# Kernel tuning notes

Hardware: AMD Instinct MI355X
Metric: run time of the kernel (lower is better)

## Reference

```python
import jax, jax.numpy as jnp
import numpy as np

N = 50000       # nodes
E = 800000      # edges (avg degree 16)
F_IN = 128      # num_node_features
H = 128         # hidden_dim
C = 16          # num_classes
G = 512         # graphs in batch


def setup_inputs() -> dict:
    key = jax.random.key(0)
    ks = jax.random.split(key, 12)
    x = jax.random.normal(ks[0], (N, F_IN), dtype=jnp.float32)
    edge_index = jax.random.randint(ks[1], (2, E), 0, N, dtype=jnp.int32)
    batch = jnp.sort(jax.random.randint(ks[2], (N,), 0, G, dtype=jnp.int32))
    def lin(k, fan_in, shape):
        bound = 1.0 / np.sqrt(fan_in)
        return jax.random.uniform(k, shape, jnp.float32, -bound, bound)
    # SAGEConv1: lin_l (aggr, with bias), lin_r (root, no bias)
    w1l = lin(ks[3], F_IN, (F_IN, H)); b1 = lin(ks[4], F_IN, (H,))
    w1r = lin(ks[5], F_IN, (F_IN, H))
    # SAGEConv2
    w2l = lin(ks[6], H, (H, H)); b2 = lin(ks[7], H, (H,))
    w2r = lin(ks[8], H, (H, H))
    # final fc
    wf = lin(ks[9], H, (H, C)); bf = lin(ks[10], H, (C,))
    return {"x": x, "edge_index": edge_index, "batch": batch,
            "w1l": w1l, "b1": b1, "w1r": w1r,
            "w2l": w2l, "b2": b2, "w2r": w2r,
            "wf": wf, "bf": bf}


def _sage_conv(x, src, dst, wl, bl, wr):
    # mean-aggregate source-node features at destination nodes
    msg_sum = jax.ops.segment_sum(x[src], dst, num_segments=N)      # [N, d]
    cnt = jax.ops.segment_sum(jnp.ones((src.shape[0], 1), x.dtype), dst,
                              num_segments=N)                        # [N, 1]
    aggr = msg_sum / jnp.maximum(cnt, 1.0)
    return aggr @ wl + bl + x @ wr


def reference(x, edge_index, batch, w1l, b1, w1r, w2l, b2, w2r, wf, bf):
    src, dst = edge_index[0], edge_index[1]
    h = jax.nn.relu(_sage_conv(x, src, dst, w1l, b1, w1r))
    # dropout(p=0.5) is identity at inference
    h = jax.nn.relu(_sage_conv(h, src, dst, w2l, b2, w2r))
    # global_mean_pool over graph ids
    gsum = jax.ops.segment_sum(h, batch, num_segments=G)             # [G, H]
    gcnt = jax.ops.segment_sum(jnp.ones((N, 1), h.dtype), batch,
                               num_segments=G)                        # [G, 1]
    g = gsum / jnp.maximum(gcnt, 1.0)
    logits = g @ wf + bf
    return jax.nn.log_softmax(logits, axis=1)
```

## Files before the change

kernel.cpp:

```cpp
#include <hip/hip_runtime.h>
#include <hip/hip_bf16.h>
#include <math.h>


#define FDIM 128

typedef __attribute__((ext_vector_type(8))) short bf16x8;
typedef __attribute__((ext_vector_type(4))) float f32x4;

__device__ inline unsigned short f2bf(float f) {
    union { float f; unsigned u; } v; v.f = f;
    unsigned r = v.u + 0x7fff + ((v.u >> 16) & 1);
    return (unsigned short)(r >> 16);
}
__device__ inline float bf2f(unsigned short b) {
    union { unsigned u; float f; } v; v.u = ((unsigned)b) << 16;
    return v.f;
}

__device__ inline void acc8(float* a, uint4 w) {
    union { unsigned u; float f; } t;
    t.u = w.x << 16;          a[0] += t.f;
    t.u = w.x & 0xffff0000u;  a[1] += t.f;
    t.u = w.y << 16;          a[2] += t.f;
    t.u = w.y & 0xffff0000u;  a[3] += t.f;
    t.u = w.z << 16;          a[4] += t.f;
    t.u = w.z & 0xffff0000u;  a[5] += t.f;
    t.u = w.w << 16;          a[6] += t.f;
    t.u = w.w & 0xffff0000u;  a[7] += t.f;
}
__device__ inline void acc8m(float* a, uint4 w, float m) {
    union { unsigned u; float f; } t;
    t.u = w.x << 16;          a[0] = fmaf(m, t.f, a[0]);
    t.u = w.x & 0xffff0000u;  a[1] = fmaf(m, t.f, a[1]);
    t.u = w.y << 16;          a[2] = fmaf(m, t.f, a[2]);
    t.u = w.y & 0xffff0000u;  a[3] = fmaf(m, t.f, a[3]);
    t.u = w.z << 16;          a[4] = fmaf(m, t.f, a[4]);
    t.u = w.z & 0xffff0000u;  a[5] = fmaf(m, t.f, a[5]);
    t.u = w.w << 16;          a[6] = fmaf(m, t.f, a[6]);
    t.u = w.w & 0xffff0000u;  a[7] = fmaf(m, t.f, a[7]);
}

__global__ __launch_bounds__(256) void prep_k(
        const int* __restrict__ dst, int* __restrict__ deg, int* __restrict__ rank, int nE,
        const float* __restrict__ x, unsigned short* __restrict__ xb, int n4,
        const float* __restrict__ w1l, const float* __restrict__ w1r,
        unsigned short* __restrict__ wp1,
        const float* __restrict__ w2l, const float* __restrict__ w2r,
        unsigned short* __restrict__ wp2,
        int nbE, int nbC) {
    int bid = blockIdx.x, tid = threadIdx.x;
    if (bid < nbE) {
        int e = bid * 256 + tid;
        if (e < nE) rank[e] = atomicAdd(&deg[dst[e]], 1);
    } else if (bid < nbE + nbC) {
        int i = (bid - nbE) * 256 + tid;
        if (i < n4) {
            float4 v = ((const float4*)x)[i];
            ushort4 o;
            o.x = f2bf(v.x); o.y = f2bf(v.y); o.z = f2bf(v.z); o.w = f2bf(v.w);
            ((ushort4*)xb)[i] = o;
        }
    } else {
        int pb = bid - nbE - nbC;
        const float* wl = (pb < 16) ? w1l : w2l;
        const float* wr = (pb < 16) ? w1r : w2r;
        unsigned short* wp = (pb < 16) ? wp1 : wp2;
        int t = (pb & 15) * 256 + tid;
        int lane = t & 63, s = (t >> 6) & 7, nt = t >> 9;
        int kbase = s * 32 + ((lane >> 4) * 8);
        int c = nt * 16 + (lane & 15);
        unsigned short tmp[8];
        #pragma unroll
        for (int j = 0; j < 8; ++j) {
            int k = kbase + j;
            float w = (k < 128) ? wl[k * 128 + c] : wr[(k - 128) * 128 + c];
            tmp[j] = f2bf(w);
        }
        ushort4 lo, hi;
        lo.x = tmp[0]; lo.y = tmp[1]; lo.z = tmp[2]; lo.w = tmp[3];
        hi.x = tmp[4]; hi.y = tmp[5]; hi.z = tmp[6]; hi.w = tmp[7];
        ((ushort4*)wp)[t * 2 + 0] = lo;
        ((ushort4*)wp)[t * 2 + 1] = hi;
    }
}

__global__ __launch_bounds__(256) void scan1_k(const int* __restrict__ deg,
                                               int* __restrict__ rowstart,
                                               int* __restrict__ bsum, int n) {
    __shared__ int s[256];
    int tid = threadIdx.x;
    int i = blockIdx.x * 256 + tid;
    int v = (i < n) ? deg[i] : 0;
    s[tid] = v;
    __syncthreads();
    for (int off = 1; off < 256; off <<= 1) {
        int t = (tid >= off) ? s[tid - off] : 0;
        __syncthreads();
        s[tid] += t;
        __syncthreads();
    }
    if (i < n) rowstart[i] = s[tid] - v;
    if (tid == 255) bsum[blockIdx.x] = s[255];
}

__global__ __launch_bounds__(256) void scan2_k(int* __restrict__ bsum, int nb) {
    __shared__ int s[256];
    int tid = threadIdx.x;
    int v = (tid < nb) ? bsum[tid] : 0;
    s[tid] = v;
    __syncthreads();
    for (int off = 1; off < 256; off <<= 1) {
        int t = (tid >= off) ? s[tid - off] : 0;
        __syncthreads();
        s[tid] += t;
        __syncthreads();
    }
    if (tid < nb) bsum[tid] = s[tid] - v;
}

__global__ void addoff_k(int* __restrict__ rowstart, const int* __restrict__ bsum, int n) {
    int i = blockIdx.x * blockDim.x + threadIdx.x;
    if (i < n) rowstart[i] += bsum[blockIdx.x];
}

__global__ __launch_bounds__(256) void fill_swz_k(
        const int* __restrict__ src, const int* __restrict__ dst,
        const int* __restrict__ rowstart, const int* __restrict__ rank,
        int* __restrict__ csr, int nE, int rngSize) {
    int cls = blockIdx.x & 7;
    int lo = cls * rngSize, hi = lo + rngSize;
    int nb = gridDim.x >> 3;
    int bi = blockIdx.x >> 3;
    for (int e = bi * 256 + threadIdx.x; e < nE; e += nb * 256) {
        int d = dst[e];
        if (d >= lo && d < hi)
            csr[rowstart[d] + rank[e]] = src[e];
    }
}

__global__ __launch_bounds__(256) void gather_v4_k(
        const uint4* __restrict__ feat,
        const int* __restrict__ csr, const int* __restrict__ rowstart,
        const int* __restrict__ deg, uint4* __restrict__ outr, int n) {
    int node = blockIdx.x * 4 + (threadIdx.x >> 6);
    if (node >= n) return;
    int lane = threadIdx.x & 63;
    int es = lane >> 4;
    int cs = lane & 15;
    int s0 = rowstart[node], dc = deg[node];

    float acc[8] = {0.f, 0.f, 0.f, 0.f, 0.f, 0.f, 0.f, 0.f};
    int base = 0;
    int i0 = 0, i1 = 0, i2 = 0, i3 = 0;
    if (base + 16 <= dc) {
        i0 = csr[s0 + es];
        i1 = csr[s0 + 4 + es];
        i2 = csr[s0 + 8 + es];
        i3 = csr[s0 + 12 + es];
    }
    while (base + 16 <= dc) {
        uint4 w0 = feat[(size_t)i0 * 16 + cs];
        uint4 w1 = feat[(size_t)i1 * 16 + cs];
        uint4 w2 = feat[(size_t)i2 * 16 + cs];
        uint4 w3 = feat[(size_t)i3 * 16 + cs];
        base += 16;
        if (base + 16 <= dc) {
            i0 = csr[s0 + base + es];
            i1 = csr[s0 + base + 4 + es];
            i2 = csr[s0 + base + 8 + es];
            i3 = csr[s0 + base + 12 + es];
        }
        acc8(acc, w0);
        acc8(acc, w1);
        acc8(acc, w2);
        acc8(acc, w3);
    }
    if (base < dc) {
        int c = dc - 1;
        int e0 = base + es, e1 = base + 4 + es, e2 = base + 8 + es, e3 = base + 12 + es;
        int t0 = csr[s0 + min(e0, c)];
        int t1 = csr[s0 + min(e1, c)];
        int t2 = csr[s0 + min(e2, c)];
        int t3 = csr[s0 + min(e3, c)];
        uint4 w0 = feat[(size_t)t0 * 16 + cs];
        uint4 w1 = feat[(size_t)t1 * 16 + cs];
        uint4 w2 = feat[(size_t)t2 * 16 + cs];
        uint4 w3 = feat[(size_t)t3 * 16 + cs];
        acc8m(acc, w0, (e0 < dc) ? 1.0f : 0.0f);
        acc8m(acc, w1, (e1 < dc) ? 1.0f : 0.0f);
        acc8m(acc, w2, (e2 < dc) ? 1.0f : 0.0f);
        acc8m(acc, w3, (e3 < dc) ? 1.0f : 0.0f);
    }

    #pragma unroll
    for (int k = 0; k < 8; ++k) {
        acc[k] += __shfl_xor(acc[k], 16, 64);
        acc[k] += __shfl_xor(acc[k], 32, 64);
    }

    if (es == 0) {
        float inv = (dc > 0) ? 1.0f / (float)dc : 0.0f;
        uint4 o;
        o.x = ((unsigned)f2bf(acc[1] * inv) << 16) | (unsigned)f2bf(acc[0] * inv);
        o.y = ((unsigned)f2bf(acc[3] * inv) << 16) | (unsigned)f2bf(acc[2] * inv);
        o.z = ((unsigned)f2bf(acc[5] * inv) << 16) | (unsigned)f2bf(acc[4] * inv);
        o.w = ((unsigned)f2bf(acc[7] * inv) << 16) | (unsigned)f2bf(acc[6] * inv);
        outr[(size_t)node * 16 + cs] = o;
    }
}

__global__ __launch_bounds__(256) void gemm_mfma_k(
        const unsigned short* __restrict__ A,
        const unsigned short* __restrict__ R,
        const unsigned short* __restrict__ wp,
        const float* __restrict__ bias,
        unsigned short* __restrict__ outp,
        int n) {
    int tid = threadIdx.x;
    int wave = tid >> 6, lane = tid & 63;
    int rowTile = blockIdx.x * 64 + wave * 16;
    int lrow = lane & 15, lk = lane >> 4;

    int arow = rowTile + lrow;
    if (arow >= n) arow = n - 1;

    bf16x8 a[8];
    const unsigned short* abase = A + (size_t)arow * FDIM + lk * 8;
    const unsigned short* rbase = R + (size_t)arow * FDIM + lk * 8;
    #pragma unroll
    for (int s = 0; s < 4; ++s) a[s] = *(const bf16x8*)(abase + s * 32);
    #pragma unroll
    for (int s = 0; s < 4; ++s) a[4 + s] = *(const bf16x8*)(rbase + s * 32);

    const bf16x8* bp = (const bf16x8*)wp;
    int ocol = lane & 15;
    int orow0 = rowTile + (lane >> 4) * 4;

    #pragma unroll
    for (int nt = 0; nt < 8; ++nt) {
        float bv = bias[nt * 16 + ocol];
        f32x4 acc = {bv, bv, bv, bv};
        #pragma unroll
        for (int s = 0; s < 8; ++s) {
            bf16x8 b = bp[(nt * 8 + s) * 64 + lane];
            acc = __builtin_amdgcn_mfma_f32_16x16x32_bf16(a[s], b, acc, 0, 0, 0);
        }
        #pragma unroll
        for (int r = 0; r < 4; ++r) {
            int orow = orow0 + r;
            if (orow < n) {
                float v = fmaxf(acc[r], 0.0f);
                outp[(size_t)orow * FDIM + nt * 16 + ocol] = f2bf(v);
            }
        }
    }
}

__global__ __launch_bounds__(256) void pool_seg_k(
        const unsigned short* __restrict__ h,
        const int* __restrict__ batch,
        float* __restrict__ gsum, int* __restrict__ gcnt, int nN) {
    __shared__ int bw[64];
    __shared__ float red[8][32][4];
    int base = blockIdx.x * 64;
    if (base >= nN) return;
    int tid = threadIdx.x;
    int rg = tid >> 5, cs = tid & 31;
    int cnt = min(64, nN - base);
    if (tid < 64) bw[tid] = batch[min(base + tid, nN - 1)];
    __syncthreads();
    int g0 = bw[0], g1 = bw[cnt - 1];

    for (int g = g0; g <= g1; ++g) {
        int s = 0;
        while (s < cnt && bw[s] < g) ++s;
        int e = s;
        while (e < cnt && bw[e] == g) ++e;

        float a0 = 0.f, a1 = 0.f, a2 = 0.f, a3 = 0.f;
        for (int i = s + rg; i < e; i += 8) {
            uint2 v = ((const uint2*)(h + (size_t)(base + i) * FDIM))[cs];
            a0 += bf2f((unsigned short)(v.x & 0xffff));
            a1 += bf2f((unsigned short)(v.x >> 16));
            a2 += bf2f((unsigned short)(v.y & 0xffff));
            a3 += bf2f((unsigned short)(v.y >> 16));
        }
        red[rg][cs][0] = a0; red[rg][cs][1] = a1;
        red[rg][cs][2] = a2; red[rg][cs][3] = a3;
        __syncthreads();
        if (rg == 0 && e > s) {
            #pragma unroll
            for (int r = 1; r < 8; ++r) {
                a0 += red[r][cs][0]; a1 += red[r][cs][1];
                a2 += red[r][cs][2]; a3 += red[r][cs][3];
            }
            float* go = gsum + (size_t)g * FDIM + cs * 4;
            atomicAdd(go + 0, a0);
            atomicAdd(go + 1, a1);
            atomicAdd(go + 2, a2);
            atomicAdd(go + 3, a3);
            if (cs == 0) atomicAdd(&gcnt[g], e - s);
        }
        __syncthreads();
    }
}

__global__ __launch_bounds__(128) void head_k(const float* __restrict__ gsum,
                                              const int* __restrict__ gcnt,
                                              const float* __restrict__ wf,
                                              const float* __restrict__ bf,
                                              float* __restrict__ out, int nG) {
    int g = blockIdx.x;
    if (g >= nG) return;
    __shared__ float row[FDIM];
    int tid = threadIdx.x;
    float inv = 1.0f / fmaxf((float)gcnt[g], 1.0f);
    row[tid] = gsum[(size_t)g * FDIM + tid] * inv;
    __syncthreads();

    float logit = -1e30f;
    if (tid < 16) {
        logit = bf[tid];
        for (int k = 0; k < FDIM; ++k) logit += row[k] * wf[k * 16 + tid];
    }
    float m = logit;
    for (int off = 8; off >= 1; off >>= 1) m = fmaxf(m, __shfl_xor(m, off, 64));
    float ev = (tid < 16) ? expf(logit - m) : 0.0f;
    float sum = ev;
    for (int off = 8; off >= 1; off >>= 1) sum += __shfl_xor(sum, off, 64);
    if (tid < 16) out[(size_t)g * 16 + tid] = logit - m - logf(sum);
}

extern "C" void kernel_launch(void* const* d_in, const int* in_sizes, int n_in,
                              void* d_out, int out_size, void* d_ws, size_t ws_size,
                              hipStream_t stream) {
    const float* x    = (const float*)d_in[0];
    const int*   ei   = (const int*)d_in[1];
    const int*   batch= (const int*)d_in[2];
    const float* w1l  = (const float*)d_in[3];
    const float* b1   = (const float*)d_in[4];
    const float* w1r  = (const float*)d_in[5];
    const float* w2l  = (const float*)d_in[6];
    const float* b2   = (const float*)d_in[7];
    const float* w2r  = (const float*)d_in[8];
    const float* wf   = (const float*)d_in[9];
    const float* bf   = (const float*)d_in[10];
    float* out = (float*)d_out;

    const int N = in_sizes[0] / FDIM;
    const int E = in_sizes[1] / 2;
    const int G = out_size / 16;
    const int* src = ei;
    const int* dst = ei + E;
    const int NB = (N + 255) / 256;

    char* ws = (char*)d_ws;
    size_t off = 0;
    auto alloc = [&](size_t bytes) { void* p = ws + off; off = (off + bytes + 255) & ~(size_t)255; return p; };
    unsigned short* xb   = (unsigned short*)alloc((size_t)N * FDIM * 2);
    unsigned short* aggr = (unsigned short*)alloc((size_t)N * FDIM * 2);
    unsigned short* h1   = (unsigned short*)alloc((size_t)N * FDIM * 2);
    unsigned short* wp1  = (unsigned short*)alloc(8 * 8 * 64 * 8 * 2);
    unsigned short* wp2  = (unsigned short*)alloc(8 * 8 * 64 * 8 * 2);
    int* deg      = (int*)alloc((size_t)N * sizeof(int));
    int* rowstart = (int*)alloc((size_t)N * sizeof(int));
    int* bsum     = (int*)alloc(256 * sizeof(int));
    int* csr      = (int*)alloc((size_t)E * sizeof(int));
    int* rank     = (int*)alloc((size_t)E * sizeof(int));
    float* gsum   = (float*)alloc((size_t)G * FDIM * sizeof(float));
    int*   gcnt   = (int*)alloc((size_t)G * sizeof(int));
    unsigned short* h2 = xb;

    hipMemsetAsync(deg, 0, (size_t)N * sizeof(int), stream);
    hipMemsetAsync(gsum, 0, (size_t)G * FDIM * sizeof(float), stream);
    hipMemsetAsync(gcnt, 0, (size_t)G * sizeof(int), stream);

    const int nbE = (E + 255) / 256;
    const int nbC = (N * FDIM / 4 + 255) / 256;
    prep_k<<<nbE + nbC + 32, 256, 0, stream>>>(dst, deg, rank, E,
                                               x, xb, N * FDIM / 4,
                                               w1l, w1r, wp1, w2l, w2r, wp2,
                                               nbE, nbC);

    scan1_k<<<NB, 256, 0, stream>>>(deg, rowstart, bsum, N);
    scan2_k<<<1, 256, 0, stream>>>(bsum, NB);
    addoff_k<<<NB, 256, 0, stream>>>(rowstart, bsum, N);
    {
        int rngSize = (N + 7) / 8;
        fill_swz_k<<<2048, 256, 0, stream>>>(src, dst, rowstart, rank, csr, E, rngSize);
    }

    gather_v4_k<<<(N + 3) / 4, 256, 0, stream>>>((const uint4*)xb, csr, rowstart, deg,
                                                 (uint4*)aggr, N);
    gemm_mfma_k<<<(N + 63) / 64, 256, 0, stream>>>(aggr, xb, wp1, b1, h1, N);

    gather_v4_k<<<(N + 3) / 4, 256, 0, stream>>>((const uint4*)h1, csr, rowstart, deg,
                                                 (uint4*)aggr, N);
    gemm_mfma_k<<<(N + 63) / 64, 256, 0, stream>>>(aggr, h1, wp2, b2, h2, N);

    pool_seg_k<<<(N + 63) / 64, 256, 0, stream>>>(h2, batch, gsum, gcnt, N);
    head_k<<<G, 128, 0, stream>>>(gsum, gcnt, wf, bf, out, G);
}
```

Before: 177.1 us.

## Build CSR with per-node atomic cursors instead of stored edge ranks

Removes the per-edge rank array: degree counting moves into a separate swizzled kernel where each block handles one destination range, and the CSR fill claims slots with atomicAdd on a per-node cursor initialised from rowstart. This drops the rank write and read and should keep atomics local to one XCD range. In exchange the degree count no longer overlaps with the x conversion in one launch, adds a kernel launch, and makes neighbour order within a row nondeterministic, so float summation order can vary between runs.

```diff
diff --git a/kernel.cpp b/kernel.cpp
--- a/kernel.cpp
+++ b/kernel.cpp
@@ -42,19 +42,15 @@
 }
 
 __global__ __launch_bounds__(256) void prep_k(
-        const int* __restrict__ dst, int* __restrict__ deg, int* __restrict__ rank, int nE,
         const float* __restrict__ x, unsigned short* __restrict__ xb, int n4,
         const float* __restrict__ w1l, const float* __restrict__ w1r,
         unsigned short* __restrict__ wp1,
         const float* __restrict__ w2l, const float* __restrict__ w2r,
         unsigned short* __restrict__ wp2,
-        int nbE, int nbC) {
+        int nbC) {
     int bid = blockIdx.x, tid = threadIdx.x;
-    if (bid < nbE) {
-        int e = bid * 256 + tid;
-        if (e < nE) rank[e] = atomicAdd(&deg[dst[e]], 1);
-    } else if (bid < nbE + nbC) {
-        int i = (bid - nbE) * 256 + tid;
+    if (bid < nbC) {
+        int i = bid * 256 + tid;
         if (i < n4) {
             float4 v = ((const float4*)x)[i];
             ushort4 o;
@@ -62,7 +58,7 @@
             ((ushort4*)xb)[i] = o;
         }
     } else {
-        int pb = bid - nbE - nbC;
+        int pb = bid - nbC;
         const float* wl = (pb < 16) ? w1l : w2l;
         const float* wr = (pb < 16) ? w1r : w2r;
         unsigned short* wp = (pb < 16) ? wp1 : wp2;
@@ -85,6 +81,18 @@
     }
 }
 
+__global__ __launch_bounds__(256) void deg_swz_k(
+        const int* __restrict__ dst, int* __restrict__ deg, int nE, int rngSize) {
+    int cls = blockIdx.x & 7;
+    int lo = cls * rngSize, hi = lo + rngSize;
+    int nb = gridDim.x >> 3;
+    int bi = blockIdx.x >> 3;
+    for (int e = bi * 256 + threadIdx.x; e < nE; e += nb * 256) {
+        int d = dst[e];
+        if (d >= lo && d < hi) atomicAdd(&deg[d], 1);
+    }
+}
+
 __global__ __launch_bounds__(256) void scan1_k(const int* __restrict__ deg,
                                                int* __restrict__ rowstart,
                                                int* __restrict__ bsum, int n) {
@@ -119,23 +127,29 @@
     if (tid < nb) bsum[tid] = s[tid] - v;
 }
 
-__global__ void addoff_k(int* __restrict__ rowstart, const int* __restrict__ bsum, int n) {
+__global__ void addoff_k(int* __restrict__ rowstart, const int* __restrict__ bsum,
+                         int* __restrict__ cursor, int n) {
     int i = blockIdx.x * blockDim.x + threadIdx.x;
-    if (i < n) rowstart[i] += bsum[blockIdx.x];
-}
-
-__global__ __launch_bounds__(256) void fill_swz_k(
+    if (i < n) {
+        int v = rowstart[i] + bsum[blockIdx.x];
+        rowstart[i] = v;
+        cursor[i] = v;
+    }
+}
+
+__global__ __launch_bounds__(256) void fill_cur_k(
         const int* __restrict__ src, const int* __restrict__ dst,
-        const int* __restrict__ rowstart, const int* __restrict__ rank,
-        int* __restrict__ csr, int nE, int rngSize) {
+        int* __restrict__ cursor, int* __restrict__ csr, int nE, int rngSize) {
     int cls = blockIdx.x & 7;
     int lo = cls * rngSize, hi = lo + rngSize;
     int nb = gridDim.x >> 3;
     int bi = blockIdx.x >> 3;
     for (int e = bi * 256 + threadIdx.x; e < nE; e += nb * 256) {
         int d = dst[e];
-        if (d >= lo && d < hi)
-            csr[rowstart[d] + rank[e]] = src[e];
+        if (d >= lo && d < hi) {
+            int p = atomicAdd(&cursor[d], 1);
+            csr[p] = src[e];
+        }
     }
 }
 
@@ -365,9 +379,9 @@
     unsigned short* wp2  = (unsigned short*)alloc(8 * 8 * 64 * 8 * 2);
     int* deg      = (int*)alloc((size_t)N * sizeof(int));
     int* rowstart = (int*)alloc((size_t)N * sizeof(int));
+    int* cursor   = (int*)alloc((size_t)N * sizeof(int));
     int* bsum     = (int*)alloc(256 * sizeof(int));
     int* csr      = (int*)alloc((size_t)E * sizeof(int));
-    int* rank     = (int*)alloc((size_t)E * sizeof(int));
     float* gsum   = (float*)alloc((size_t)G * FDIM * sizeof(float));
     int*   gcnt   = (int*)alloc((size_t)G * sizeof(int));
     unsigned short* h2 = xb;
@@ -376,20 +390,17 @@
     hipMemsetAsync(gsum, 0, (size_t)G * FDIM * sizeof(float), stream);
     hipMemsetAsync(gcnt, 0, (size_t)G * sizeof(int), stream);
 
-    const int nbE = (E + 255) / 256;
+    const int rngSize = (N + 7) / 8;
+
     const int nbC = (N * FDIM / 4 + 255) / 256;
-    prep_k<<<nbE + nbC + 32, 256, 0, stream>>>(dst, deg, rank, E,
-                                               x, xb, N * FDIM / 4,
-                                               w1l, w1r, wp1, w2l, w2r, wp2,
-                                               nbE, nbC);
+    prep_k<<<nbC + 32, 256, 0, stream>>>(x, xb, N * FDIM / 4,
+                                         w1l, w1r, wp1, w2l, w2r, wp2, nbC);
+    deg_swz_k<<<2048, 256, 0, stream>>>(dst, deg, E, rngSize);
 
     scan1_k<<<NB, 256, 0, stream>>>(deg, rowstart, bsum, N);
     scan2_k<<<1, 256, 0, stream>>>(bsum, NB);
-    addoff_k<<<NB, 256, 0, stream>>>(rowstart, bsum, N);
-    {
-        int rngSize = (N + 7) / 8;
-        fill_swz_k<<<2048, 256, 0, stream>>>(src, dst, rowstart, rank, csr, E, rngSize);
-    }
+    addoff_k<<<NB, 256, 0, stream>>>(rowstart, bsum, cursor, N);
+    fill_cur_k<<<2048, 256, 0, stream>>>(src, dst, cursor, csr, E, rngSize);
 
     gather_v4_k<<<(N + 3) / 4, 256, 0, stream>>>((const uint4*)xb, csr, rowstart, deg,
                                                  (uint4*)aggr, N);
```

New measurement: 205.5 us. +16.0%, slower.
